# Optimization experiments

Hardware: AMD Instinct MI355X
Metric: run time of the kernel (lower is better)

Reference implementation:

```python
import jax, jax.numpy as jnp
import numpy as np

B, T, NE, H = 4, 1024, 1024, 16
HS = NE // H  # 64
EPS = 0.00064


def setup_inputs() -> dict:
    key = jax.random.key(0)
    ks = jax.random.split(key, 30)
    def rn(k, shape, s):
        return jax.random.normal(k, shape, jnp.float32) * s
    d = {}
    d["x"] = jax.random.normal(ks[0], (B, T, NE), jnp.float32)
    d["time_maa_x"] = jax.random.uniform(ks[1], (NE,), jnp.float32)
    d["time_maa"] = jax.random.uniform(ks[2], (4, 1, 1, NE), jnp.float32)
    d["maa_w1"] = rn(ks[3], (128, NE), 0.02)   # 4 * D_MIX_LORA=32
    d["maa_w2"] = rn(ks[4], (4, 32, NE), 0.02)
    d["decay_w1"] = rn(ks[5], (64, NE), 0.02)
    d["decay_w2"] = rn(ks[6], (64, NE), 0.02)
    d["aaa_w1"] = rn(ks[7], (16, NE), 0.02)
    d["aaa_w2"] = rn(ks[8], (16, NE), 0.02)
    d["kkk_w1"] = rn(ks[9], (16, NE), 0.02)
    d["kkk_w2"] = rn(ks[10], (16, NE), 0.02)
    d["gate_w1"] = rn(ks[11], (128, NE), 0.02)
    d["gate_w2"] = rn(ks[12], (128, NE), 0.02)
    d["ma_w1"] = rn(ks[13], (16, NE), 0.02)
    d["ma_w2"] = rn(ks[14], (16, NE), 0.02)
    d["mk_w1"] = rn(ks[15], (16, NE), 0.02)
    d["mk_w2"] = rn(ks[16], (16, NE), 0.02)
    d["time_decay"] = jnp.linspace(-6.5, -1.5, NE, dtype=jnp.float32)  # decay_speed + 0.5 shape
    d["time_faaaa"] = rn(ks[17], (NE,), 0.02)
    d["time_aaaaa"] = rn(ks[18], (NE,), 0.02)
    d["time_misc_a"] = rn(ks[19], (NE,), 0.02)
    d["time_misc_k"] = rn(ks[20], (NE,), 0.02)
    d["Wr"] = rn(ks[21], (NE, NE), 0.5 / NE ** 0.5)
    d["Wk"] = rn(ks[22], (NE, NE), 0.05 / NE ** 0.5)
    d["Wv"] = rn(ks[23], (NE, NE), 0.5 / NE ** 0.5)
    d["Wo"] = rn(ks[24], (NE, NE), 1.0 / NE ** 0.5)
    d["ln_w"] = jnp.ones((NE,), jnp.float32)
    d["ln_b"] = jnp.zeros((NE,), jnp.float32)
    return d


def _forward(x, time_maa_x, time_maa, maa_w1, maa_w2, decay_w1, decay_w2,
             aaa_w1, aaa_w2, kkk_w1, kkk_w2, gate_w1, gate_w2,
             ma_w1, ma_w2, mk_w1, mk_w2, time_decay, time_faaaa, time_aaaaa,
             time_misc_a, time_misc_k, Wr, Wk, Wv, Wo, ln_w, ln_b):
    Bx, Tx, C = x.shape
    # token-shift delta: xx[t] = x[t-1] - x[t], with x[-1] = 0
    xx = jnp.pad(x, ((0, 0), (1, 0), (0, 0)))[:, :Tx] - x
    mix = x + xx * time_maa_x
    lo = jnp.tanh(jnp.einsum('btc,dc->btd', mix, maa_w1)).reshape(Bx, Tx, 4, 32)
    lo = jnp.einsum('btgk,gkc->gbtc', lo, maa_w2)           # [4,B,T,C]
    xm = x[None] + xx[None] * (lo + time_maa)               # time_maa broadcasts [4,1,1,C]
    xrg, xwa, xk, xv = xm[0], xm[1], xm[2], xm[3]

    r = xrg @ Wr.T
    g = jnp.tanh(xrg @ gate_w1.T) @ gate_w2
    k = xk @ Wk.T
    v = xv @ Wv.T
    w2 = jnp.tanh(xwa @ decay_w1.T) @ decay_w2
    w = -jax.nn.softplus(-(time_decay + w2)) - 0.5
    kk = k + jnp.tanh(xk @ kkk_w1.T) @ kkk_w2
    kkh = kk.reshape(Bx, Tx, H, HS)
    kk = (kkh / jnp.maximum(jnp.linalg.norm(kkh, axis=-1, keepdims=True), 1e-12)).reshape(Bx, Tx, C)
    a = jax.nn.sigmoid(time_aaaaa + (xwa @ aaa_w1.T) @ aaa_w2)
    ma = jax.nn.sigmoid(time_misc_a + (xwa @ ma_w1.T) @ ma_w2)
    k = k * ma + k * a * (1.0 - ma)
    mk = jax.nn.sigmoid(time_misc_k + (xk @ mk_w1.T) @ mk_w2)
    k = k * jnp.exp(w * mk)
    b = -kk * a

    # RWKV7 delta-rule recurrence: per-(B,H) HSxHS matrix state, scan over T
    def to_th(t):
        return t.reshape(Bx, Tx, H, HS).transpose(1, 0, 2, 3)  # [T,B,H,HS]
    qt, wt, kt, vt, at, bt = map(to_th, (r, w, k, v, kk, b))
    wt = jnp.exp(-jnp.exp(wt))

    def step(s, inp):
        q_, w_, k_, v_, a_, b_ = inp
        sa = jnp.einsum('bhij,bhj->bhi', s, a_)
        s = s * w_[:, :, None, :] + sa[..., None] * b_[:, :, None, :] + v_[..., None] * k_[:, :, None, :]
        return s, jnp.einsum('bhij,bhj->bhi', s, q_)

    s0 = jnp.zeros((Bx, H, HS, HS), x.dtype)
    _, y = jax.lax.scan(step, s0, (qt, wt, kt, vt, at, bt))
    y = y.transpose(1, 0, 2, 3).reshape(Bx, Tx, C)

    # GroupNorm with H groups, eps=0.00064
    yg = y.reshape(Bx, Tx, H, HS)
    mu = yg.mean(-1, keepdims=True)
    var = ((yg - mu) ** 2).mean(-1, keepdims=True)
    y = ((yg - mu) / jnp.sqrt(var + EPS)).reshape(Bx, Tx, C) * ln_w + ln_b

    # per-head bonus: (r.k * faaaa) v
    rk = (r.reshape(Bx, Tx, H, HS) * k.reshape(Bx, Tx, H, HS) * time_faaaa.reshape(H, HS)).sum(-1, keepdims=True)
    y = y + (rk * v.reshape(Bx, Tx, H, HS)).reshape(Bx, Tx, C)
    return (y * g) @ Wo.T


def reference(x, time_maa_x, time_maa, maa_w1, maa_w2, decay_w1, decay_w2,
              aaa_w1, aaa_w2, kkk_w1, kkk_w2, gate_w1, gate_w2,
              ma_w1, ma_w2, mk_w1, mk_w2, time_decay, time_faaaa, time_aaaaa,
              time_misc_a, time_misc_k, Wr, Wk, Wv, Wo, ln_w, ln_b):
    return _forward(x, time_maa_x, time_maa, maa_w1, maa_w2, decay_w1, decay_w2,
                    aaa_w1, aaa_w2, kkk_w1, kkk_w2, gate_w1, gate_w2,
                    ma_w1, ma_w2, mk_w1, mk_w2, time_decay, time_faaaa, time_aaaaa,
                    time_misc_a, time_misc_k, Wr, Wk, Wv, Wo, ln_w, ln_b)
```

## Files before the change

kernel.cpp:

```cpp
#include <hip/hip_runtime.h>
#include <cstdint>
#include <cstddef>

#define BB   4
#define TT   1024
#define CC   1024
#define HH   16
#define HSS  64
#define NNtok 4096
#define EPSGN 0.00064f
#define W2TS 192

typedef unsigned short bf16u;
typedef __attribute__((ext_vector_type(8))) short short8;
typedef __attribute__((ext_vector_type(4))) float f32x4;
#define SLOT 4194304ull

__device__ __forceinline__ float bf2f(bf16u u){
  union { unsigned int i; float f; } cv; cv.i = ((unsigned int)u) << 16; return cv.f;
}
__device__ __forceinline__ unsigned short f2bfbits(unsigned int x){
  return (unsigned short)((x + 0x7fffu + ((x >> 16) & 1u)) >> 16);
}
__device__ __forceinline__ bf16u f2bf(float f){
  union { float f; unsigned int i; } cv; cv.f = f;
  return f2bfbits(cv.i);
}
__device__ __forceinline__ void ld4bf(const bf16u* p, float* o){
  ushort4 u = *reinterpret_cast<const ushort4*>(p);
  o[0]=bf2f(u.x); o[1]=bf2f(u.y); o[2]=bf2f(u.z); o[3]=bf2f(u.w);
}
__device__ __forceinline__ void st4bf(bf16u* p, const float* v){
  ushort4 u; u.x=f2bf(v[0]); u.y=f2bf(v[1]); u.z=f2bf(v[2]); u.w=f2bf(v[3]);
  *reinterpret_cast<ushort4*>(p) = u;
}
__device__ __forceinline__ unsigned short f2h(float f){
  union { _Float16 h; unsigned short s; } c; c.h = (_Float16)f; return c.s;
}
__device__ __forceinline__ void st4h(bf16u* p, const float* v){
  ushort4 u; u.x=f2h(v[0]); u.y=f2h(v[1]); u.z=f2h(v[2]); u.w=f2h(v[3]);
  *reinterpret_cast<ushort4*>(p) = u;
}
__device__ __forceinline__ void ld4f(const float* p, float* o){
  float4 v = *reinterpret_cast<const float4*>(p);
  o[0]=v.x; o[1]=v.y; o[2]=v.z; o[3]=v.w;
}
__device__ __forceinline__ float sigm(float x){ return 1.f / (1.f + expf(-x)); }

__device__ __forceinline__ float bflo(unsigned int u){
  union { unsigned int i; float f; } c; c.i = u << 16; return c.f;
}
__device__ __forceinline__ float bfhi(unsigned int u){
  union { unsigned int i; float f; } c; c.i = u & 0xffff0000u; return c.f;
}
__device__ __forceinline__ float hlo(unsigned int u){
  union { unsigned short s; _Float16 h; } c; c.s = (unsigned short)(u & 0xffffu); return (float)c.h;
}
__device__ __forceinline__ float hhi(unsigned int u){
  union { unsigned short s; _Float16 h; } c; c.s = (unsigned short)(u >> 16); return (float)c.h;
}
__device__ __forceinline__ float hval(unsigned short s){
  union { unsigned short s; _Float16 h; } c; c.s = s; return (float)c.h;
}
__device__ __forceinline__ float dot4(const float* x, const float* y){
  return (x[0]*y[0] + x[1]*y[1]) + (x[2]*y[2] + x[3]*y[3]);
}

__device__ __forceinline__ void gload_lds16(const bf16u* g, short* l){
  __builtin_amdgcn_global_load_lds(
      (const __attribute__((address_space(1))) unsigned int*)g,
      (__attribute__((address_space(3))) unsigned int*)l,
      16, 0, 0);
}

template<int CTRL>
__device__ __forceinline__ float dpp_add(float v){
  union { float f; int i; } a, b;
  a.f = v;
  b.i = __builtin_amdgcn_update_dpp(0, a.i, CTRL, 0xF, 0xF, true);
  return v + b.f;
}
__device__ __forceinline__ float red16(float v){
  v = dpp_add<0xB1>(v);
  v = dpp_add<0x4E>(v);
  v = dpp_add<0x124>(v);
  v = dpp_add<0x128>(v);
  return v;
}
__device__ __forceinline__ float red32(float v){
  v = red16(v);
  union { float f; int i; } x, y;
  x.f = v; y.f = v;
  asm volatile("" : "+v"(y.i));
  asm volatile("v_permlane16_swap_b32 %0, %1" : "+v"(x.i), "+v"(y.i));
  return x.f + y.f;
}

__global__ __launch_bounds__(256) void k_prep(const float* __restrict__ x,
                                              const float* __restrict__ tmx,
                                              bf16u* __restrict__ MIX){
  int e = (blockIdx.x * 256 + threadIdx.x) * 4;
  int n = e >> 10;
  int c = e & (CC - 1);
  int t = n & (TT - 1);
  float xf[4]; ld4f(x + e, xf);
  float pf[4] = {0.f, 0.f, 0.f, 0.f};
  if (t > 0) ld4f(x + e - CC, pf);
  float tm[4]; ld4f(tmx + c, tm);
  float mv[4];
  #pragma unroll
  for (int i = 0; i < 4; ++i) mv[i] = xf[i] + (pf[i] - xf[i]) * tm[i];
  st4bf(MIX + e, mv);
}

__global__ __launch_bounds__(256) void k_prep_wconv(
    const float* __restrict__ x, const float* __restrict__ tmx,
    bf16u* __restrict__ MIX,
    const float* __restrict__ Wr, const float* __restrict__ Wk,
    const float* __restrict__ Wv,
    const float* __restrict__ maa_w1, const float* __restrict__ gate_w1,
    const float* __restrict__ decay_w1, const float* __restrict__ aaa_w1,
    const float* __restrict__ ma_w1, const float* __restrict__ kkk_w1,
    const float* __restrict__ mk_w1,
    const float* __restrict__ maa_w2, const float* __restrict__ decay_w2,
    bf16u* __restrict__ WrB, bf16u* __restrict__ WkB, bf16u* __restrict__ WvB,
    bf16u* __restrict__ W1B, bf16u* __restrict__ W2TB){
  int tid = threadIdx.x;
  if (blockIdx.x < 4096){
    int e = (blockIdx.x * 256 + tid) * 4;
    int n = e >> 10;
    int c = e & (CC - 1);
    int t = n & (TT - 1);
    float xf[4]; ld4f(x + e, xf);
    float pf[4] = {0.f, 0.f, 0.f, 0.f};
    if (t > 0) ld4f(x + e - CC, pf);
    float tm[4]; ld4f(tmx + c, tm);
    float mv[4];
    #pragma unroll
    for (int i = 0; i < 4; ++i) mv[i] = xf[i] + (pf[i] - xf[i]) * tm[i];
    st4bf(MIX + e, mv);
    return;
  }
  int blk = blockIdx.x - 4096;
  if (blk < 3072){
    const float* src = (blk < 1024) ? Wr : (blk < 2048) ? Wk : Wv;
    bf16u* dst = (blk < 1024) ? WrB : (blk < 2048) ? WkB : WvB;
    size_t e = (size_t)(blk & 1023) * 1024 + (size_t)tid * 4;
    float v[4]; ld4f(src + e, v);
    st4bf(dst + e, v);
  } else if (blk < 3456){
    int row = blk - 3072;
    const float* src;
    if      (row < 128) src = maa_w1   + (size_t)row * 1024;
    else if (row < 256) src = gate_w1  + (size_t)(row - 128) * 1024;
    else if (row < 320) src = decay_w1 + (size_t)(row - 256) * 1024;
    else if (row < 336) src = aaa_w1   + (size_t)(row - 320) * 1024;
    else if (row < 352) src = ma_w1    + (size_t)(row - 336) * 1024;
    else if (row < 368) src = kkk_w1   + (size_t)(row - 352) * 1024;
    else                src = mk_w1    + (size_t)(row - 368) * 1024;
    float v[4]; ld4f(src + tid * 4, v);
    st4bf(W1B + (size_t)row * 1024 + tid * 4, v);
  } else {
    int j = blk - 3456;
    const float* src = (j < 128) ? (maa_w2 + (size_t)j * 1024)
                                 : (decay_w2 + (size_t)(j - 128) * 1024);
    for (int c = tid; c < 1024; c += 256)
      W2TB[(size_t)c * W2TS + j] = f2bf(src[c]);
  }
}

#define B64_AROW 72
#define B64_ASZ (64*72)
#define B64_BSZ (128*72)
template<bool OB>
__device__ __forceinline__ void gemm_b64_body(const bf16u* __restrict__ X,
                                              const bf16u* __restrict__ WB,
                                              void* __restrict__ OUTv,
                                              int Nd, int Kd, int act_n,
                                              short* __restrict__ As,
                                              short* __restrict__ Bs,
                                              int bn0, int bm0){
  const int tid  = threadIdx.x;
  const int lane = tid & 63;
  const int wv   = tid >> 6;
  const int wm   = wv >> 1, wn = wv & 1;
  const int l15  = lane & 15;
  const int quad = lane >> 4;

  f32x4 acc[2][4];
  #pragma unroll
  for (int mi = 0; mi < 2; ++mi)
    #pragma unroll
    for (int ni = 0; ni < 4; ++ni)
      #pragma unroll
      for (int rg = 0; rg < 4; ++rg) acc[mi][ni][rg] = 0.f;

  const int ra = tid >> 2, k0a = (tid & 3) * 16;
  const int rb = tid >> 1, k0b = (tid & 1) * 32;
  const bf16u* xsrc = X + (size_t)(bm0 + ra) * Kd;
  const bf16u* wsrc = (bn0 + rb < Nd) ? WB + (size_t)(bn0 + rb) * Kd : nullptr;

  uint4 xa0 = *(const uint4*)(xsrc + k0a);
  uint4 xa1 = *(const uint4*)(xsrc + k0a + 8);
  uint4 wa0 = make_uint4(0,0,0,0), wa1 = wa0, wa2 = wa0, wa3 = wa0;
  if (wsrc){
    wa0 = *(const uint4*)(wsrc + k0b);
    wa1 = *(const uint4*)(wsrc + k0b + 8);
    wa2 = *(const uint4*)(wsrc + k0b + 16);
    wa3 = *(const uint4*)(wsrc + k0b + 24);
  }
  *(uint4*)&As[ra * B64_AROW + k0a]      = xa0;
  *(uint4*)&As[ra * B64_AROW + k0a + 8]  = xa1;
  *(uint4*)&Bs[rb * B64_AROW + k0b]      = wa0;
  *(uint4*)&Bs[rb * B64_AROW + k0b + 8]  = wa1;
  *(uint4*)&Bs[rb * B64_AROW + k0b + 16] = wa2;
  *(uint4*)&Bs[rb * B64_AROW + k0b + 24] = wa3;
  __syncthreads();

  const int NS = Kd >> 6;
  for (int s = 0; s < NS; ++s){
    const int cur = s & 1;
    if (s + 1 < NS){
      int kb = (s + 1) << 6;
      xa0 = *(const uint4*)(xsrc + kb + k0a);
      xa1 = *(const uint4*)(xsrc + kb + k0a + 8);
      if (wsrc){
        wa0 = *(const uint4*)(wsrc + kb + k0b);
        wa1 = *(const uint4*)(wsrc + kb + k0b + 8);
        wa2 = *(const uint4*)(wsrc + kb + k0b + 16);
        wa3 = *(const uint4*)(wsrc + kb + k0b + 24);
      }
    }
    #pragma unroll
    for (int kk = 0; kk < 64; kk += 32){
      short8 af[2], bfg[4];
      #pragma unroll
      for (int mi = 0; mi < 2; ++mi)
        af[mi] = *(const short8*)&As[cur*B64_ASZ + (wm*32 + mi*16 + l15) * B64_AROW + kk + quad*8];
      #pragma unroll
      for (int ni = 0; ni < 4; ++ni)
        bfg[ni] = *(const short8*)&Bs[cur*B64_BSZ + (wn*64 + ni*16 + l15) * B64_AROW + kk + quad*8];
      #pragma unroll
      for (int mi = 0; mi < 2; ++mi)
        #pragma unroll
        for (int ni = 0; ni < 4; ++ni)
          acc[mi][ni] = __builtin_amdgcn_mfma_f32_16x16x32_bf16(af[mi], bfg[ni], acc[mi][ni], 0, 0, 0);
    }
    if (s + 1 < NS){
      const int nxt = cur ^ 1;
      *(uint4*)&As[nxt*B64_ASZ + ra * B64_AROW + k0a]      = xa0;
      *(uint4*)&As[nxt*B64_ASZ + ra * B64_AROW + k0a + 8]  = xa1;
      *(uint4*)&Bs[nxt*B64_BSZ + rb * B64_AROW + k0b]      = wa0;
      *(uint4*)&Bs[nxt*B64_BSZ + rb * B64_AROW + k0b + 8]  = wa1;
      *(uint4*)&Bs[nxt*B64_BSZ + rb * B64_AROW + k0b + 16] = wa2;
      *(uint4*)&Bs[nxt*B64_BSZ + rb * B64_AROW + k0b + 24] = wa3;
      __syncthreads();
    }
  }

  #pragma unroll
  for (int mi = 0; mi < 2; ++mi){
    #pragma unroll
    for (int ni = 0; ni < 4; ++ni){
      int col = bn0 + wn*64 + ni*16 + l15;
      if (col >= Nd) continue;
      #pragma unroll
      for (int rg = 0; rg < 4; ++rg){
        int row = bm0 + wm*32 + mi*16 + quad*4 + rg;
        float v = acc[mi][ni][rg];
        if (col < act_n) v = tanhf(v);
        if (OB) ((bf16u*)OUTv)[(size_t)row * Nd + col] = f2bf(v);
        else    ((float*)OUTv)[(size_t)row * Nd + col] = v;
      }
    }
  }
}

template<bool OB>
__global__ __launch_bounds__(256) void k_gemm_b64(const bf16u* __restrict__ X,
                                                  const bf16u* __restrict__ WB,
                                                  void* __restrict__ OUTv,
                                                  int Nd, int Kd, int act_n){
  __shared__ short As[2*B64_ASZ];
  __shared__ short Bs[2*B64_BSZ];
  gemm_b64_body<OB>(X, WB, OUTv, Nd, Kd, act_n, As, Bs,
                    blockIdx.x * 128, blockIdx.y * 64);
}

#define B128L_SZ (128*32)
template<bool OB>
__device__ __forceinline__ void gemm_b128_lds_body(const bf16u* __restrict__ X,
                                                   const bf16u* __restrict__ WB,
                                                   void* __restrict__ OUTv,
                                                   int Nd, int Kd, int act_n,
                                                   short* __restrict__ As,
                                                   short* __restrict__ Bs,
                                                   int bn0, int bm0){
  const int tid  = threadIdx.x;
  const int lane = tid & 63;
  const int wv   = tid >> 6;
  const int wm   = wv >> 1, wn = wv & 1;
  const int l15  = lane & 15;
  const int quad = lane >> 4;

  f32x4 acc[4][4];
  #pragma unroll
  for (int mi = 0; mi < 4; ++mi)
    #pragma unroll
    for (int ni = 0; ni < 4; ++ni)
      #pragma unroll
      for (int rg = 0; rg < 4; ++rg) acc[mi][ni][rg] = 0.f;

  const int srow = lane >> 2;
  const int cl   = (lane & 3) ^ ((lane >> 3) & 3);
  const bf16u* gA0 = X  + (size_t)(bm0 + wv*32 + srow)      * Kd + cl*8;
  const bf16u* gA1 = X  + (size_t)(bm0 + wv*32 + 16 + srow) * Kd + cl*8;
  const bf16u* gB0 = WB + (size_t)(bn0 + wv*32 + srow)      * Kd + cl*8;
  const bf16u* gB1 = WB + (size_t)(bn0 + wv*32 + 16 + srow) * Kd + cl*8;
  short* ldsA0 = As + wv*1024;
  short* ldsA1 = As + wv*1024 + 512;
  short* ldsB0 = Bs + wv*1024;
  short* ldsB1 = Bs + wv*1024 + 512;

  gload_lds16(gA0, ldsA0);
  gload_lds16(gA1, ldsA1);
  gload_lds16(gB0, ldsB0);
  gload_lds16(gB1, ldsB1);
  __syncthreads();

  const int cq = (quad ^ ((l15 >> 1) & 3)) * 8;
  const int NK = Kd >> 5;
  for (int k = 0; k < NK; ++k){
    const int cur = k & 1;
    if (k + 1 < NK){
      int ko = (k + 1) << 5;
      const int nxt = cur ^ 1;
      gload_lds16(gA0 + ko, ldsA0 + nxt*B128L_SZ);
      gload_lds16(gA1 + ko, ldsA1 + nxt*B128L_SZ);
      gload_lds16(gB0 + ko, ldsB0 + nxt*B128L_SZ);
      gload_lds16(gB1 + ko, ldsB1 + nxt*B128L_SZ);
    }
    short8 af[4], bfg[4];
    #pragma unroll
    for (int mi = 0; mi < 4; ++mi)
      af[mi] = *(const short8*)&As[cur*B128L_SZ + (wm*64 + mi*16 + l15) * 32 + cq];
    #pragma unroll
    for (int ni = 0; ni < 4; ++ni)
      bfg[ni] = *(const short8*)&Bs[cur*B128L_SZ + (wn*64 + ni*16 + l15) * 32 + cq];
    #pragma unroll
    for (int mi = 0; mi < 4; ++mi)
      #pragma unroll
      for (int ni = 0; ni < 4; ++ni)
        acc[mi][ni] = __builtin_amdgcn_mfma_f32_16x16x32_bf16(af[mi], bfg[ni], acc[mi][ni], 0, 0, 0);
    if (k + 1 < NK)
      __syncthreads();
  }

  #pragma unroll
  for (int mi = 0; mi < 4; ++mi){
    #pragma unroll
    for (int ni = 0; ni < 4; ++ni){
      int col = bn0 + wn*64 + ni*16 + l15;
      if (col >= Nd) continue;
      #pragma unroll
      for (int rg = 0; rg < 4; ++rg){
        int row = bm0 + wm*64 + mi*16 + quad*4 + rg;
        float v = acc[mi][ni][rg];
        if (col < act_n) v = tanhf(v);
        if (OB) ((bf16u*)OUTv)[(size_t)row * Nd + col] = f2bf(v);
        else    ((float*)OUTv)[(size_t)row * Nd + col] = v;
      }
    }
  }
}

__global__ __launch_bounds__(256) void k_gemm_b128_rkv(const bf16u* __restrict__ X0,
                                                       const bf16u* __restrict__ X2,
                                                       const bf16u* __restrict__ X3,
                                                       const bf16u* __restrict__ WrB,
                                                       const bf16u* __restrict__ WkB,
                                                       const bf16u* __restrict__ WvB,
                                                       bf16u* __restrict__ R,
                                                       bf16u* __restrict__ K0,
                                                       bf16u* __restrict__ V){
  __shared__ short As[2*B128L_SZ];
  __shared__ short Bs[2*B128L_SZ];
  const int z = blockIdx.z;
  const int bn0 = blockIdx.x * 128, bm0 = blockIdx.y * 128;
  if (z == 0)      gemm_b128_lds_body<true>(X0, WrB, R,  CC, CC, 0, As, Bs, bn0, bm0);
  else if (z == 1) gemm_b128_lds_body<true>(X2, WkB, K0, CC, CC, 0, As, Bs, bn0, bm0);
  else             gemm_b128_lds_body<true>(X3, WvB, V,  CC, CC, 0, As, Bs, bn0, bm0);
}

__global__ __launch_bounds__(256) void k_gemm_b64_lora(const bf16u* __restrict__ X0,
                                                       const bf16u* __restrict__ X1,
                                                       const bf16u* __restrict__ X2,
                                                       const bf16u* __restrict__ W1B,
                                                       bf16u* __restrict__ GT,
                                                       bf16u* __restrict__ P1,
                                                       bf16u* __restrict__ P2){
  __shared__ short As[2*B64_ASZ];
  __shared__ short Bs[2*B64_BSZ];
  const int z = blockIdx.z;
  const int bm0 = blockIdx.y * 64;
  if (z == 0)
    gemm_b64_body<true>(X0, W1B + 128*1024, GT, 128, CC, 128, As, Bs, 0, bm0);
  else if (z == 1)
    gemm_b64_body<true>(X1, W1B + 256*1024, P1, 96, CC, 64, As, Bs, 0, bm0);
  else
    gemm_b64_body<true>(X2, W1B + 352*1024, P2, 32, CC, 16, As, Bs, 0, bm0);
}

template<int KD, int EP>
__device__ __forceinline__ void gemm_nn_body(const bf16u* __restrict__ A, int lda,
                                             const bf16u* __restrict__ BT, int koff,
                                             bf16u* __restrict__ OUT,
                                             const float* __restrict__ x,
                                             const float* __restrict__ tma_g,
                                             short* __restrict__ As,
                                             short* __restrict__ Bs,
                                             int bn0, int bm0){
  const int tid  = threadIdx.x;
  const int lane = tid & 63;
  const int wv   = tid >> 6;
  const int wm   = wv >> 1, wn = wv & 1;
  const int l15  = lane & 15;
  const int quad = lane >> 4;

  for (int idx = tid; idx < 128 * (KD / 8); idx += 256){
    int r  = idx / (KD / 8);
    int kc = (idx % (KD / 8)) * 8;
    *(uint4*)&As[r * (KD + 8) + kc] =
        *(const uint4*)(A + (size_t)(bm0 + r) * lda + kc);
  }
  for (int idx = tid; idx < 128 * (KD / 8); idx += 256){
    int cc_ = idx / (KD / 8);
    int kc  = (idx % (KD / 8)) * 8;
    *(uint4*)&Bs[cc_ * (KD + 8) + kc] =
        *(const uint4*)(BT + (size_t)(bn0 + cc_) * W2TS + koff + kc);
  }
  __syncthreads();

  f32x4 acc[4][4];
  #pragma unroll
  for (int mi = 0; mi < 4; ++mi)
    #pragma unroll
    for (int ni = 0; ni < 4; ++ni)
      #pragma unroll
      for (int rg = 0; rg < 4; ++rg) acc[mi][ni][rg] = 0.f;

  #pragma unroll
  for (int kk = 0; kk < KD; kk += 32){
    short8 af[4], bfg[4];
    #pragma unroll
    for (int mi = 0; mi < 4; ++mi)
      af[mi] = *(const short8*)&As[(wm*64 + mi*16 + l15) * (KD + 8) + kk + quad*8];
    #pragma unroll
    for (int ni = 0; ni < 4; ++ni)
      bfg[ni] = *(const short8*)&Bs[(wn*64 + ni*16 + l15) * (KD + 8) + kk + quad*8];
    #pragma unroll
    for (int mi = 0; mi < 4; ++mi)
      #pragma unroll
      for (int ni = 0; ni < 4; ++ni)
        acc[mi][ni] = __builtin_amdgcn_mfma_f32_16x16x32_bf16(af[mi], bfg[ni], acc[mi][ni], 0, 0, 0);
  }

  #pragma unroll
  for (int mi = 0; mi < 4; ++mi){
    #pragma unroll
    for (int ni = 0; ni < 4; ++ni){
      int col = bn0 + wn*64 + ni*16 + l15;
      float tm = (EP == 1) ? tma_g[col] : 0.f;
      #pragma unroll
      for (int rg = 0; rg < 4; ++rg){
        int row = bm0 + wm*64 + mi*16 + quad*4 + rg;
        float v = acc[mi][ni][rg];
        if (EP == 1){
          float xv = x[(size_t)row * CC + col];
          float xp = ((row & (TT - 1)) == 0) ? 0.f : x[(size_t)row * CC + col - CC];
          v = xv + (xp - xv) * (v + tm);
        }
        OUT[(size_t)row * CC + col] = f2bf(v);
      }
    }
  }
}

template<int KD, int EP>
__global__ __launch_bounds__(256) void k_gemm_nn_b(const bf16u* __restrict__ A, int lda,
                                                   const bf16u* __restrict__ BT, int koff,
                                                   bf16u* __restrict__ OUT,
                                                   const float* __restrict__ x,
                                                   const float* __restrict__ tma_g){
  __shared__ short As[128 * (KD + 8)];
  __shared__ short Bs[128 * (KD + 8)];
  gemm_nn_body<KD, EP>(A, lda, BT, koff, OUT, x, tma_g, As, Bs,
                       blockIdx.x * 128, blockIdx.y * 128);
}

__global__ __launch_bounds__(256) void k_gemm_nn_b4(const bf16u* __restrict__ LO,
                                                    const bf16u* __restrict__ BT,
                                                    bf16u* __restrict__ X0base,
                                                    const float* __restrict__ x,
                                                    const float* __restrict__ tmaa){
  __shared__ short As[128 * 40];
  __shared__ short Bs[128 * 40];
  const int z = blockIdx.z;
  gemm_nn_body<32, 1>(LO + z*32, 128, BT, z*32, X0base + (size_t)z*SLOT,
                      x, tmaa + (size_t)z*CC, As, Bs,
                      blockIdx.x * 128, blockIdx.y * 128);
}

template<bool OB>
__global__ __launch_bounds__(256) void k_gemm_mfma(const bf16u* __restrict__ X,
                                                   const float* __restrict__ Wa,
                                                   const float* __restrict__ Wb,
                                                   const float* __restrict__ Wc,
                                                   int na, int nab,
                                                   void* __restrict__ OUTv,
                                                   int Nd, int Kd, int act_n){
  __shared__ short As[128 * 40];
  __shared__ short Bs[128 * 40];
  const int tid  = threadIdx.x;
  const int lane = tid & 63;
  const int wv   = tid >> 6;
  const int wm   = wv >> 1, wn = wv & 1;
  const int bn0  = blockIdx.x * 128;
  const int bm0  = blockIdx.y * 128;
  const int l15  = lane & 15;
  const int quad = lane >> 4;

  f32x4 acc[4][4];
  #pragma unroll
  for (int mi = 0; mi < 4; ++mi)
    #pragma unroll
    for (int ni = 0; ni < 4; ++ni)
      #pragma unroll
      for (int rg = 0; rg < 4; ++rg) acc[mi][ni][rg] = 0.f;

  const int r    = tid >> 1;
  const int half = (tid & 1) * 16;

  int rr = bn0 + r;
  const float* wsrc = nullptr;
  if (rr < na)        wsrc = Wa + (size_t)rr * Kd;
  else if (rr < nab)  wsrc = Wb + (size_t)(rr - na) * Kd;
  else if (rr < Nd)   wsrc = Wc + (size_t)(rr - nab) * Kd;
  const bf16u* xsrc = X + (size_t)(bm0 + r) * Kd;

  for (int k0 = 0; k0 < Kd; k0 += 32){
    uint4 xa = *(const uint4*)(xsrc + k0 + half);
    uint4 xb = *(const uint4*)(xsrc + k0 + half + 8);
    uint4 w0 = make_uint4(0,0,0,0), w1 = w0, w2 = w0, w3 = w0;
    if (wsrc){
      w0 = *(const uint4*)(wsrc + k0 + half);
      w1 = *(const uint4*)(wsrc + k0 + half + 4);
      w2 = *(const uint4*)(wsrc + k0 + half + 8);
      w3 = *(const uint4*)(wsrc + k0 + half + 12);
    }
    union { unsigned short s[8]; uint4 v; } p0, p1;
    p0.s[0]=f2bfbits(w0.x); p0.s[1]=f2bfbits(w0.y); p0.s[2]=f2bfbits(w0.z); p0.s[3]=f2bfbits(w0.w);
    p0.s[4]=f2bfbits(w1.x); p0.s[5]=f2bfbits(w1.y); p0.s[6]=f2bfbits(w1.z); p0.s[7]=f2bfbits(w1.w);
    p1.s[0]=f2bfbits(w2.x); p1.s[1]=f2bfbits(w2.y); p1.s[2]=f2bfbits(w2.z); p1.s[3]=f2bfbits(w2.w);
    p1.s[4]=f2bfbits(w3.x); p1.s[5]=f2bfbits(w3.y); p1.s[6]=f2bfbits(w3.z); p1.s[7]=f2bfbits(w3.w);

    *(uint4*)&As[r * 40 + half]     = xa;
    *(uint4*)&As[r * 40 + half + 8] = xb;
    *(uint4*)&Bs[r * 40 + half]     = p0.v;
    *(uint4*)&Bs[r * 40 + half + 8] = p1.v;
    __syncthreads();

    short8 af[4], bfg[4];
    #pragma unroll
    for (int mi = 0; mi < 4; ++mi)
      af[mi] = *(const short8*)&As[(wm*64 + mi*16 + l15) * 40 + quad*8];
    #pragma unroll
    for (int ni = 0; ni < 4; ++ni)
      bfg[ni] = *(const short8*)&Bs[(wn*64 + ni*16 + l15) * 40 + quad*8];
    #pragma unroll
    for (int mi = 0; mi < 4; ++mi)
      #pragma unroll
      for (int ni = 0; ni < 4; ++ni)
        acc[mi][ni] = __builtin_amdgcn_mfma_f32_16x16x32_bf16(af[mi], bfg[ni], acc[mi][ni], 0, 0, 0);
    __syncthreads();
  }

  #pragma unroll
  for (int mi = 0; mi < 4; ++mi){
    #pragma unroll
    for (int ni = 0; ni < 4; ++ni){
      int col = bn0 + wn*64 + ni*16 + l15;
      if (col >= Nd) continue;
      #pragma unroll
      for (int rg = 0; rg < 4; ++rg){
        int row = bm0 + wm*64 + mi*16 + quad*4 + rg;
        float v = acc[mi][ni][rg];
        if (col < act_n) v = tanhf(v);
        if (OB) ((bf16u*)OUTv)[(size_t)row * Nd + col] = f2bf(v);
        else    ((float*)OUTv)[(size_t)row * Nd + col] = v;
      }
    }
  }
}

template<int KD, int EP>
__global__ __launch_bounds__(256) void k_gemm_nn(const bf16u* __restrict__ A, int lda,
                                                 const float* __restrict__ B,
                                                 bf16u* __restrict__ OUT,
                                                 const float* __restrict__ x,
                                                 const float* __restrict__ tma_g){
  __shared__ short As[128 * (KD + 8)];
  __shared__ short Bs[128 * (KD + 8)];
  const int tid  = threadIdx.x;
  const int lane = tid & 63;
  const int wv   = tid >> 6;
  const int wm   = wv >> 1, wn = wv & 1;
  const int bn0  = blockIdx.x * 128;
  const int bm0  = blockIdx.y * 128;
  const int l15  = lane & 15;
  const int quad = lane >> 4;

  for (int idx = tid; idx < 128 * (KD / 8); idx += 256){
    int r  = idx / (KD / 8);
    int kc = (idx % (KD / 8)) * 8;
    *(uint4*)&As[r * (KD + 8) + kc] =
        *(const uint4*)(A + (size_t)(bm0 + r) * lda + kc);
  }
  for (int idx = tid; idx < KD * 128; idx += 256){
    int k = idx >> 7, c = idx & 127;
    Bs[c * (KD + 8) + k] = (short)f2bf(B[(size_t)k * CC + bn0 + c]);
  }
  __syncthreads();

  f32x4 acc[4][4];
  #pragma unroll
  for (int mi = 0; mi < 4; ++mi)
    #pragma unroll
    for (int ni = 0; ni < 4; ++ni)
      #pragma unroll
      for (int rg = 0; rg < 4; ++rg) acc[mi][ni][rg] = 0.f;

  #pragma unroll
  for (int kk = 0; kk < KD; kk += 32){
    short8 af[4], bfg[4];
    #pragma unroll
    for (int mi = 0; mi < 4; ++mi)
      af[mi] = *(const short8*)&As[(wm*64 + mi*16 + l15) * (KD + 8) + kk + quad*8];
    #pragma unroll
    for (int ni = 0; ni < 4; ++ni)
      bfg[ni] = *(const short8*)&Bs[(wn*64 + ni*16 + l15) * (KD + 8) + kk + quad*8];
    #pragma unroll
    for (int mi = 0; mi < 4; ++mi)
      #pragma unroll
      for (int ni = 0; ni < 4; ++ni)
        acc[mi][ni] = __builtin_amdgcn_mfma_f32_16x16x32_bf16(af[mi], bfg[ni], acc[mi][ni], 0, 0, 0);
  }

  #pragma unroll
  for (int mi = 0; mi < 4; ++mi){
    #pragma unroll
    for (int ni = 0; ni < 4; ++ni){
      int col = bn0 + wn*64 + ni*16 + l15;
      float tm = (EP == 1) ? tma_g[col] : 0.f;
      #pragma unroll
      for (int rg = 0; rg < 4; ++rg){
        int row = bm0 + wm*64 + mi*16 + quad*4 + rg;
        float v = acc[mi][ni][rg];
        if (EP == 1){
          float xv = x[(size_t)row * CC + col];
          float xp = ((row & (TT - 1)) == 0) ? 0.f : x[(size_t)row * CC + col - CC];
          v = xv + (xp - xv) * (v + tm);
        }
        OUT[(size_t)row * CC + col] = f2bf(v);
      }
    }
  }
}

template<int WMODE>
__global__ __launch_bounds__(256) void k_elem(bf16u* __restrict__ K0,
    const bf16u* __restrict__ P1, const bf16u* __restrict__ P2,
    const bf16u* __restrict__ W2A,
    const float* __restrict__ kw2, const float* __restrict__ aw2,
    const float* __restrict__ maw2, const float* __restrict__ mkw2,
    const float* __restrict__ td,  const float* __restrict__ taa,
    const float* __restrict__ tma, const float* __restrict__ tmk,
    const float* __restrict__ faaaa,
    bf16u* __restrict__ KKN, bf16u* __restrict__ Bb, bf16u* __restrict__ UX,
    float* __restrict__ WF,
    bf16u* __restrict__ Rq, float* __restrict__ Dsc, float* __restrict__ RKsc,
    const float* __restrict__ Wo, const float* __restrict__ gate_w2,
    bf16u* __restrict__ WoB, bf16u* __restrict__ GW2T){
  int tid = threadIdx.x;
  if (blockIdx.x >= 1024){
    int blk = blockIdx.x - 1024;
    if (blk < 1024){
      size_t e = ((size_t)blk * 256 + tid) * 4;
      float v[4]; ld4f(Wo + e, v);
      st4bf(WoB + e, v);
    } else {
      int c = (blk - 1024) * 2 + (tid >> 7);
      int j = tid & 127;
      GW2T[(size_t)c * 128 + j] = f2bf(gate_w2[(size_t)j * CC + c]);
    }
    return;
  }
  int n0 = blockIdx.x * 4;
  __shared__ float at_l[4][16], mat_l[4][16], kt_l[4][16], mkt_l[4][16];
  {
    int grp = tid >> 6, q = tid & 63, tt = q >> 4, j = q & 15;
    if (grp == 0)      at_l[tt][j]  = bf2f(P1[(size_t)(n0+tt)*96 + 64 + j]);
    else if (grp == 1) mat_l[tt][j] = bf2f(P1[(size_t)(n0+tt)*96 + 80 + j]);
    else if (grp == 2) kt_l[tt][j]  = bf2f(P2[(size_t)(n0+tt)*32 + j]);
    else               mkt_l[tt][j] = bf2f(P2[(size_t)(n0+tt)*32 + 16 + j]);
  }
  __syncthreads();
  int c  = tid * 4;
  int h  = tid >> 4;
  int lg = tid & 15;

  float kkk[4][4], aa[4][4], mam[4][4], mkm[4][4];
  #pragma unroll
  for (int tt = 0; tt < 4; ++tt)
    #pragma unroll
    for (int i = 0; i < 4; ++i){ kkk[tt][i]=0; aa[tt][i]=0; mam[tt][i]=0; mkm[tt][i]=0; }

  #pragma unroll 4
  for (int j = 0; j < 16; ++j){
    float wk[4], wa[4], wm[4], wq[4];
    ld4f(kw2  + (size_t)j*CC + c, wk);
    ld4f(aw2  + (size_t)j*CC + c, wa);
    ld4f(maw2 + (size_t)j*CC + c, wm);
    ld4f(mkw2 + (size_t)j*CC + c, wq);
    #pragma unroll
    for (int tt = 0; tt < 4; ++tt){
      float s1 = kt_l[tt][j], s2 = at_l[tt][j], s3 = mat_l[tt][j], s4 = mkt_l[tt][j];
      #pragma unroll
      for (int i = 0; i < 4; ++i){
        kkk[tt][i] += s1 * wk[i];
        aa[tt][i]  += s2 * wa[i];
        mam[tt][i] += s3 * wm[i];
        mkm[tt][i] += s4 * wq[i];
      }
    }
  }

  float td4[4], taa4[4], tma4[4], tmk4[4], fa4[4];
  ld4f(td + c, td4); ld4f(taa + c, taa4); ld4f(tma + c, tma4); ld4f(tmk + c, tmk4);
  ld4f(faaaa + c, fa4);

#define ELEM_TOKEN(TT_, E_, A_, B_, KF_, WD_) do{ \
    float k0a[4]; ld4bf(K0 + (E_), k0a); \
    float w2a[4]; ld4bf(W2A + (E_), w2a); \
    float ssq = 0.f; \
    _Pragma("unroll") \
    for (int i = 0; i < 4; ++i){ A_[i] = k0a[i] + kkk[TT_][i]; ssq += A_[i]*A_[i]; } \
    ssq = red16(ssq); \
    float rinv = 1.f / fmaxf(sqrtf(ssq), 1e-12f); \
    float outw_[4]; \
    _Pragma("unroll") \
    for (int i = 0; i < 4; ++i){ \
      float z  = td4[i] + w2a[i]; \
      float nz = -z; \
      float sp = (nz > 15.f) ? nz : log1pf(expf(nz)); \
      float w  = -sp - 0.5f; \
      float av  = sigm(taa4[i] + aa[TT_][i]); \
      float mav = sigm(tma4[i] + mam[TT_][i]); \
      float mkv = sigm(tmk4[i] + mkm[TT_][i]); \
      A_[i] *= rinv; \
      B_[i]  = -A_[i] * av; \
      KF_[i] = k0a[i] * (mav + av * (1.f - mav)) * expf(w * mkv); \
      float ou = -expf(w); \
      outw_[i] = ou; \
      if (WMODE == 1) WD_[i] = __expf(ou);               \
      else            WD_[i] = __expf(hval(f2h(ou)));    \
    } \
    st4bf(Bb + (E_), B_); \
    st4bf(K0 + (E_), KF_); \
    if (WMODE == 1) *(float4*)(WF + (E_)) = make_float4(WD_[0], WD_[1], WD_[2], WD_[3]); \
    else            st4h(UX + (E_), outw_); \
  }while(0)

  #pragma unroll
  for (int p = 0; p < 2; ++p){
    const int ttE = 2*p, ttO = ttE + 1;
    size_t eE = (size_t)(n0 + ttE) * CC + c;
    size_t eO = eE + CC;
    float aE[4], bE[4], kfE[4], wdE[4];
    float aO[4], bO[4], kfO[4], wdO[4];
    ELEM_TOKEN(ttE, eE, aE, bE, kfE, wdE);
    ELEM_TOKEN(ttO, eO, aO, bO, kfO, wdO);
    st4bf(KKN + eE, aE);

    float rE[4], rO[4];
    ld4bf(Rq + eE, rE); ld4bf(Rq + eO, rO);

    float rkE = red16(rE[0]*kfE[0]*fa4[0] + rE[1]*kfE[1]*fa4[1]
                    + rE[2]*kfE[2]*fa4[2] + rE[3]*kfE[3]*fa4[3]);
    float rkO = red16(rO[0]*kfO[0]*fa4[0] + rO[1]*kfO[1]*fa4[1]
                    + rO[2]*kfO[2]*fa4[2] + rO[3]*kfO[3]*fa4[3]);

    float c1 = red16(dot4(bE, aO));
    float d  = red16(dot4(kfE, aO));
    float u1[4];
    #pragma unroll
    for (int i = 0; i < 4; ++i) u1[i] = wdE[i]*aO[i] + c1*aE[i];
    st4bf(KKN + eO, u1);

    float cq = red16(dot4(bE, rE));
    float e1 = red16(dot4(kfE, rE));
    float qe[4];
    #pragma unroll
    for (int i = 0; i < 4; ++i) qe[i] = wdE[i]*rE[i] + cq*aE[i];
    st4bf(Rq + eE, qe);

    float cz  = red16(dot4(bO, rO));
    float e21 = red16(dot4(kfO, rO));
    float z[4];
    #pragma unroll
    for (int i = 0; i < 4; ++i) z[i] = wdO[i]*rO[i] + cz*aO[i];
    float cy  = red16(dot4(bE, z));
    float e20 = red16(dot4(kfE, z));
    float qo[4];
    #pragma unroll
    for (int i = 0; i < 4; ++i) qo[i] = wdE[i]*z[i] + cy*aE[i];
    st4bf(Rq + eO, qo);

    if (lg == 0){
      size_t pr = (size_t)((n0 + ttE) >> 1);
      float4 dv; dv.x = d; dv.y = e1; dv.z = e20; dv.w = e21;
      *(float4*)(Dsc + (pr * HH + h) * 4) = dv;
      RKsc[(size_t)(n0 + ttE) * HH + h] = rkE;
      RKsc[(size_t)(n0 + ttO) * HH + h] = rkO;
    }
  }
#undef ELEM_TOKEN
}

template<int WMODE>
__global__ __launch_bounds__(256) void k_rec(const bf16u* __restrict__ Qp,
                                             const bf16u* __restrict__ WT,
                                             const float* __restrict__ WF,
                                             const bf16u* __restrict__ KFt,
                                             const bf16u* __restrict__ Vt,
                                             const bf16u* __restrict__ Aa,
                                             const bf16u* __restrict__ Bv,
                                             const float* __restrict__ Dsc,
                                             bf16u* __restrict__ Y){
  const int p   = blockIdx.x;
  const int g   = (p & 7) | ((p >> 6) << 3);
  const int oct = (p >> 3) & 7;
  const int b   = g >> 4;
  const int h   = g & 15;
  const int tid = threadIdx.x;
  const int l31 = tid & 31;
  const int i   = oct * 8 + (tid >> 5);
  const size_t base0 = (size_t)(b * TT) * CC + h * HSS;
  const size_t colb  = base0 + l31 * 2;
  const size_t rowb  = base0 + i;
  const size_t dscb  = ((size_t)(b * (TT/2)) * HH + h) * 4;

  float S0 = 0.f, S1 = 0.f;

  unsigned int qEA,qOA,aEA,uOA,kEA,kOA,bEA,bOA,wEA,wOA; float2 fEA,fOA; unsigned short vEA,vOA; float4 dA;
  unsigned int qEB,qOB,aEB,uOB,kEB,kOB,bEB,bOB,wEB,wOB; float2 fEB,fOB; unsigned short vEB,vOB; float4 dB;
  unsigned int qEC,qOC,aEC,uOC,kEC,kOC,bEC,bOC,wEC,wOC; float2 fEC,fOC; unsigned short vEC,vOC; float4 dC;
  unsigned int qED,qOD,aED,uOD,kED,kOD,bED,bOD,wED,wOD; float2 fED,fOD; unsigned short vED,vOD; float4 dD;

#define PL(S, T_) do{ \
    size_t cE_ = colb + (size_t)(T_) * CC, cO_ = cE_ + CC; \
    qE##S = *(const unsigned int*)(Qp  + cE_); qO##S = *(const unsigned int*)(Qp  + cO_); \
    aE##S = *(const unsigned int*)(Aa  + cE_); uO##S = *(const unsigned int*)(Aa  + cO_); \
    kE##S = *(const unsigned int*)(KFt + cE_); kO##S = *(const unsigned int*)(KFt + cO_); \
    bE##S = *(const unsigned int*)(Bv  + cE_); bO##S = *(const unsigned int*)(Bv  + cO_); \
    if (WMODE == 1){ \
      fE##S = *(const float2*)(WF + cE_); fO##S = *(const float2*)(WF + cO_); \
    } else { \
      wE##S = *(const unsigned int*)(WT + cE_); wO##S = *(const unsigned int*)(WT + cO_); \
    } \
    vE##S = Vt[rowb + (size_t)(T_) * CC]; \
    vO##S = Vt[rowb + (size_t)(T_ + 1) * CC]; \
    d##S  = *(const float4*)(Dsc + dscb + (size_t)((T_) >> 1) * (HH*4)); \
  }while(0)

#define PSTEP(S, T_) do{ \
    float a0=bflo(aE##S), a1=bfhi(aE##S); \
    float u0=bflo(uO##S), u1=bfhi(uO##S); \
    float g0=bflo(qE##S), g1=bfhi(qE##S); \
    float o0=bflo(qO##S), o1=bfhi(qO##S); \
    float pE_ = fmaf(S1, a1, S0 * a0); \
    float pO_ = fmaf(S1, u1, S0 * u0); \
    float yE_ = fmaf(S1, g1, S0 * g0); \
    float yO_ = fmaf(S1, o1, S0 * o0); \
    pE_ = red32(pE_); \
    pO_ = red32(pO_); \
    yE_ = red32(yE_); \
    yO_ = red32(yO_); \
    float vEf = bf2f(vE##S), vOf = bf2f(vO##S); \
    float saE = pE_; \
    float saO = fmaf(d##S.x, vEf, pO_); \
    float ypE = fmaf(d##S.y, vEf, yE_); \
    float ypO = fmaf(d##S.z, vEf, fmaf(d##S.w, vOf, yO_)); \
    float k0=bflo(kE##S), k1=bfhi(kE##S); \
    float b0=bflo(bE##S), b1=bfhi(bE##S); \
    float w0, w1; \
    if (WMODE == 1){ w0=fE##S.x; w1=fE##S.y; } \
    else { w0=__expf(hlo(wE##S)); w1=__expf(hhi(wE##S)); } \
    S0 = fmaf(S0, w0, fmaf(saE, b0, vEf * k0)); \
    S1 = fmaf(S1, w1, fmaf(saE, b1, vEf * k1)); \
    float ko0=bflo(kO##S), ko1=bfhi(kO##S); \
    float bo0=bflo(bO##S), bo1=bfhi(bO##S); \
    float wo0, wo1; \
    if (WMODE == 1){ wo0=fO##S.x; wo1=fO##S.y; } \
    else { wo0=__expf(hlo(wO##S)); wo1=__expf(hhi(wO##S)); } \
    S0 = fmaf(S0, wo0, fmaf(saO, bo0, vOf * ko0)); \
    S1 = fmaf(S1, wo1, fmaf(saO, bo1, vOf * ko1)); \
    if (l31 == 0){ \
      Y[rowb + (size_t)(T_) * CC]     = f2bf(ypE); \
      Y[rowb + (size_t)(T_ + 1) * CC] = f2bf(ypO); \
    } \
  }while(0)

  PL(A, 0); PL(B, 2); PL(C, 4); PL(D, 6);
  for (int t = 0; t < TT; t += 8){
    PSTEP(A, t);
    if (t + 8  < TT) PL(A, t + 8);
    PSTEP(B, t + 2);
    if (t + 10 < TT) PL(B, t + 10);
    PSTEP(C, t + 4);
    if (t + 12 < TT) PL(C, t + 12);
    PSTEP(D, t + 6);
    if (t + 14 < TT) PL(D, t + 14);
  }
#undef PL
#undef PSTEP
}

__global__ __launch_bounds__(256) void k_post(const bf16u* __restrict__ Y,
                                              const bf16u* __restrict__ Vt,
                                              const bf16u* __restrict__ GV,
                                              const float* __restrict__ lnw,
                                              const float* __restrict__ lnb,
                                              const float* __restrict__ RKsc,
                                              bf16u* __restrict__ YG){
  int n = blockIdx.x, tid = threadIdx.x;
  int c = tid * 4;
  size_t e = (size_t)n * CC + c;

  float ya[4]; ld4bf(Y + e, ya);
  float s = ya[0] + ya[1] + ya[2] + ya[3];
  s = red16(s);
  float mu = s * (1.f / 64.f);
  float d[4], vs = 0.f;
  #pragma unroll
  for (int i = 0; i < 4; ++i){ d[i] = ya[i] - mu; vs += d[i] * d[i]; }
  vs = red16(vs);
  float rstd = rsqrtf(vs * (1.f / 64.f) + EPSGN);

  float rk = RKsc[(size_t)n * HH + (tid >> 4)];

  float va[4]; ld4bf(Vt + e, va);
  float lw4[4], lb4[4];
  ld4f(lnw + c, lw4); ld4f(lnb + c, lb4);
  float g[4]; ld4bf(GV + e, g);
  float o[4];
  #pragma unroll
  for (int i = 0; i < 4; ++i){
    float yn = d[i] * rstd * lw4[i] + lb4[i] + rk * va[i];
    o[i] = yn * g[i];
  }
  st4bf(YG + e, o);
}

extern "C" void kernel_launch(void* const* d_in, const int* in_sizes, int n_in,
                              void* d_out, int out_size, void* d_ws, size_t ws_size,
                              hipStream_t stream){
  (void)in_sizes; (void)n_in; (void)out_size;
  const float* x        = (const float*)d_in[0];
  const float* tmx      = (const float*)d_in[1];
  const float* tmaa     = (const float*)d_in[2];
  const float* maa_w1   = (const float*)d_in[3];
  const float* maa_w2   = (const float*)d_in[4];
  const float* decay_w1 = (const float*)d_in[5];
  const float* decay_w2 = (const float*)d_in[6];
  const float* aaa_w1   = (const float*)d_in[7];
  const float* aaa_w2   = (const float*)d_in[8];
  const float* kkk_w1   = (const float*)d_in[9];
  const float* kkk_w2   = (const float*)d_in[10];
  const float* gate_w1  = (const float*)d_in[11];
  const float* gate_w2  = (const float*)d_in[12];
  const float* ma_w1    = (const float*)d_in[13];
  const float* ma_w2    = (const float*)d_in[14];
  const float* mk_w1    = (const float*)d_in[15];
  const float* mk_w2    = (const float*)d_in[16];
  const float* t_decay  = (const float*)d_in[17];
  const float* t_faaaa  = (const float*)d_in[18];
  const float* t_aaaaa  = (const float*)d_in[19];
  const float* t_misc_a = (const float*)d_in[20];
  const float* t_misc_k = (const float*)d_in[21];
  const float* Wr       = (const float*)d_in[22];
  const float* Wk       = (const float*)d_in[23];
  const float* Wv       = (const float*)d_in[24];
  const float* Wo       = (const float*)d_in[25];
  const float* ln_w     = (const float*)d_in[26];
  const float* ln_b     = (const float*)d_in[27];

  bf16u* bw  = (bf16u*)d_ws;
  bf16u* MIX = bw + 0*SLOT;
  bf16u* X0  = bw + 0*SLOT;
  bf16u* KKN = bw + 0*SLOT;
  bf16u* YG  = bw + 0*SLOT;
  bf16u* X1  = bw + 1*SLOT;
  bf16u* Bb  = bw + 1*SLOT;
  bf16u* GV  = bw + 1*SLOT;
  bf16u* X2  = bw + 2*SLOT;
  bf16u* UX  = bw + 2*SLOT;
  bf16u* X3  = bw + 3*SLOT;
  bf16u* W2A = bw + 3*SLOT;
  bf16u* Yb  = bw + 3*SLOT;
  bf16u* R   = bw + 4*SLOT;
  bf16u* K0  = bw + 5*SLOT;
  bf16u* V   = bw + 6*SLOT;
  char*  wsb = (char*)d_ws;
  bf16u* LO  = (bf16u*)(wsb + (56ull<<20));
  bf16u* GT  = (bf16u*)(wsb + (57ull<<20));
  bf16u* P1  = (bf16u*)(wsb + (58ull<<20));
  bf16u* P2  = (bf16u*)(wsb + (58ull<<20) + (768ull<<10));
  float* Dsc = (float*)(wsb + (59ull<<20));
  float* RKsc= (float*)(wsb + (59ull<<20) + (512ull<<10));
  float* WF  = (float*)(wsb + (60ull<<20));
  bf16u* WrB = (bf16u*)(wsb + (60ull<<20));
  bf16u* WkB = (bf16u*)(wsb + (62ull<<20));
  bf16u* WvB = (bf16u*)(wsb + (64ull<<20));
  bf16u* W1B = (bf16u*)(wsb + (66ull<<20));
  bf16u* W2TB= (bf16u*)(wsb + (67ull<<20));
  bf16u* WoB = UX;
  bf16u* GW2T= UX + 1048576;
  const bool fast = ws_size >= (77ull<<20);

  if (fast){
    k_prep_wconv<<<7744, 256, 0, stream>>>(x, tmx, MIX,
                                           Wr, Wk, Wv, maa_w1, gate_w1, decay_w1,
                                           aaa_w1, ma_w1, kkk_w1, mk_w1,
                                           maa_w2, decay_w2,
                                           WrB, WkB, WvB, W1B, W2TB);
    k_gemm_b64<true><<<dim3(1,64),256,0,stream>>>(MIX, W1B, LO, 128, CC, 128);
    k_gemm_nn_b4<<<dim3(8,32,4),256,0,stream>>>(LO, W2TB, X0, x, tmaa);
    k_gemm_b128_rkv<<<dim3(8,32,3),256,0,stream>>>(X0, X2, X3, WrB, WkB, WvB,
                                                   R, K0, V);
    k_gemm_b64_lora<<<dim3(1,64,3),256,0,stream>>>(X0, X1, X2, W1B, GT, P1, P2);
    k_gemm_nn_b<64,0><<<dim3(8,32),256,0,stream>>>(P1, 96, W2TB, 128, W2A, nullptr, nullptr);
    k_elem<1><<<2560, 256, 0, stream>>>(K0, P1, P2, W2A,
                                        kkk_w2, aaa_w2, ma_w2, mk_w2,
                                        t_decay, t_aaaaa, t_misc_a, t_misc_k, t_faaaa,
                                        KKN, Bb, UX, WF, R, Dsc, RKsc,
                                        Wo, gate_w2, WoB, GW2T);
    k_rec<1><<<512, 256, 0, stream>>>(R, UX, WF, K0, V, KKN, Bb, Dsc, Yb);
    k_gemm_b64<true><<<dim3(8,64),256,0,stream>>>(GT, GW2T, GV, CC, 128, 0);
    k_post<<<4096, 256, 0, stream>>>(Yb, V, GV, ln_w, ln_b, RKsc, YG);
    k_gemm_b64<false><<<dim3(8,64),256,0,stream>>>(YG, WoB, d_out, CC, CC, 0);
  } else {
    k_prep<<<4096, 256, 0, stream>>>(x, tmx, MIX);
    k_gemm_mfma<true><<<dim3(1,32),256,0,stream>>>(MIX, maa_w1, maa_w1, maa_w1,
                                                   128, 128, LO, 128, CC, 128);
    bf16u* XMs[4] = {X0, X1, X2, X3};
    for (int g = 0; g < 4; ++g)
      k_gemm_nn<32,1><<<dim3(8,32),256,0,stream>>>(LO + g*32, 128,
                                                   maa_w2 + (size_t)g*32*CC,
                                                   XMs[g], x, tmaa + (size_t)g*CC);
    k_gemm_mfma<true><<<dim3(8,32),256,0,stream>>>(X0, Wr, Wr, Wr, CC, CC, R,  CC, CC, 0);
    k_gemm_mfma<true><<<dim3(8,32),256,0,stream>>>(X2, Wk, Wk, Wk, CC, CC, K0, CC, CC, 0);
    k_gemm_mfma<true><<<dim3(8,32),256,0,stream>>>(X3, Wv, Wv, Wv, CC, CC, V,  CC, CC, 0);
    k_gemm_mfma<true><<<dim3(1,32),256,0,stream>>>(X0, gate_w1, gate_w1, gate_w1,
                                                   128, 128, GT, 128, CC, 128);
    k_gemm_mfma<true><<<dim3(1,32),256,0,stream>>>(X1, decay_w1, aaa_w1, ma_w1,
                                                   64, 80, P1, 96, CC, 64);
    k_gemm_mfma<true><<<dim3(1,32),256,0,stream>>>(X2, kkk_w1, mk_w1, mk_w1,
                                                   16, 32, P2, 32, CC, 16);
    k_gemm_nn<64,0><<<dim3(8,32),256,0,stream>>>(P1, 96, decay_w2, W2A, nullptr, nullptr);
    k_elem<0><<<1024, 256, 0, stream>>>(K0, P1, P2, W2A,
                                        kkk_w2, aaa_w2, ma_w2, mk_w2,
                                        t_decay, t_aaaaa, t_misc_a, t_misc_k, t_faaaa,
                                        KKN, Bb, UX, WF, R, Dsc, RKsc,
                                        Wo, gate_w2, WoB, GW2T);
    k_rec<0><<<512, 256, 0, stream>>>(R, UX, WF, K0, V, KKN, Bb, Dsc, Yb);
    k_gemm_nn<128,0><<<dim3(8,32),256,0,stream>>>(GT, 128, gate_w2, GV, nullptr, nullptr);
    k_post<<<4096, 256, 0, stream>>>(Yb, V, GV, ln_w, ln_b, RKsc, YG);
    k_gemm_mfma<false><<<dim3(8,32),256,0,stream>>>(YG, Wo, Wo, Wo, CC, CC, d_out, CC, CC, 0);
  }
}
```

Before: 571.9 us.

## Co-schedule gate GEMM with recurrence kernel in a single launch

```diff
diff --git a/kernel.cpp b/kernel.cpp
--- a/kernel.cpp
+++ b/kernel.cpp
@@ -838,16 +838,16 @@
 }
 
 template<int WMODE>
-__global__ __launch_bounds__(256) void k_rec(const bf16u* __restrict__ Qp,
-                                             const bf16u* __restrict__ WT,
-                                             const float* __restrict__ WF,
-                                             const bf16u* __restrict__ KFt,
-                                             const bf16u* __restrict__ Vt,
-                                             const bf16u* __restrict__ Aa,
-                                             const bf16u* __restrict__ Bv,
-                                             const float* __restrict__ Dsc,
-                                             bf16u* __restrict__ Y){
-  const int p   = blockIdx.x;
+__device__ __forceinline__ void krec_body(int p,
+                                          const bf16u* __restrict__ Qp,
+                                          const bf16u* __restrict__ WT,
+                                          const float* __restrict__ WF,
+                                          const bf16u* __restrict__ KFt,
+                                          const bf16u* __restrict__ Vt,
+                                          const bf16u* __restrict__ Aa,
+                                          const bf16u* __restrict__ Bv,
+                                          const float* __restrict__ Dsc,
+                                          bf16u* __restrict__ Y){
   const int g   = (p & 7) | ((p >> 6) << 3);
   const int oct = (p >> 3) & 7;
   const int b   = g >> 4;
@@ -936,6 +936,41 @@
 #undef PSTEP
 }
 
+template<int WMODE>
+__global__ __launch_bounds__(256) void k_rec(const bf16u* __restrict__ Qp,
+                                             const bf16u* __restrict__ WT,
+                                             const float* __restrict__ WF,
+                                             const bf16u* __restrict__ KFt,
+                                             const bf16u* __restrict__ Vt,
+                                             const bf16u* __restrict__ Aa,
+                                             const bf16u* __restrict__ Bv,
+                                             const float* __restrict__ Dsc,
+                                             bf16u* __restrict__ Y){
+  krec_body<WMODE>(blockIdx.x, Qp, WT, WF, KFt, Vt, Aa, Bv, Dsc, Y);
+}
+
+__global__ __launch_bounds__(256) void k_rec_gv(const bf16u* __restrict__ Qp,
+                                                const float* __restrict__ WF,
+                                                const bf16u* __restrict__ KFt,
+                                                const bf16u* __restrict__ Vt,
+                                                const bf16u* __restrict__ Aa,
+                                                const bf16u* __restrict__ Bv,
+                                                const float* __restrict__ Dsc,
+                                                bf16u* __restrict__ Y,
+                                                const bf16u* __restrict__ GT,
+                                                const bf16u* __restrict__ GW2T,
+                                                bf16u* __restrict__ GVX){
+  __shared__ short As[2*B128L_SZ];
+  __shared__ short Bs[2*B128L_SZ];
+  if (blockIdx.x < 512){
+    krec_body<1>(blockIdx.x, Qp, nullptr, WF, KFt, Vt, Aa, Bv, Dsc, Y);
+  } else {
+    const int q = blockIdx.x - 512;
+    gemm_b128_lds_body<true>(GT, GW2T, GVX, CC, 128, 0, As, Bs,
+                             (q & 7) * 128, (q >> 3) * 128);
+  }
+}
+
 __global__ __launch_bounds__(256) void k_post(const bf16u* __restrict__ Y,
                                               const bf16u* __restrict__ Vt,
                                               const bf16u* __restrict__ GV,
@@ -1036,7 +1071,9 @@
   bf16u* W2TB= (bf16u*)(wsb + (67ull<<20));
   bf16u* WoB = UX;
   bf16u* GW2T= UX + 1048576;
-  const bool fast = ws_size >= (77ull<<20);
+  bf16u* GVX = (bf16u*)(wsb + (77ull<<20));
+  const bool fast  = ws_size >= (77ull<<20);
+  const bool fast2 = ws_size >= (85ull<<20);
 
   if (fast){
     k_prep_wconv<<<7744, 256, 0, stream>>>(x, tmx, MIX,
@@ -1055,9 +1092,15 @@
                                         t_decay, t_aaaaa, t_misc_a, t_misc_k, t_faaaa,
                                         KKN, Bb, UX, WF, R, Dsc, RKsc,
                                         Wo, gate_w2, WoB, GW2T);
-    k_rec<1><<<512, 256, 0, stream>>>(R, UX, WF, K0, V, KKN, Bb, Dsc, Yb);
-    k_gemm_b64<true><<<dim3(8,64),256,0,stream>>>(GT, GW2T, GV, CC, 128, 0);
-    k_post<<<4096, 256, 0, stream>>>(Yb, V, GV, ln_w, ln_b, RKsc, YG);
+    if (fast2){
+      k_rec_gv<<<768, 256, 0, stream>>>(R, WF, K0, V, KKN, Bb, Dsc, Yb,
+                                        GT, GW2T, GVX);
+      k_post<<<4096, 256, 0, stream>>>(Yb, V, GVX, ln_w, ln_b, RKsc, YG);
+    } else {
+      k_rec<1><<<512, 256, 0, stream>>>(R, nullptr, WF, K0, V, KKN, Bb, Dsc, Yb);
+      k_gemm_b64<true><<<dim3(8,64),256,0,stream>>>(GT, GW2T, GV, CC, 128, 0);
+      k_post<<<4096, 256, 0, stream>>>(Yb, V, GV, ln_w, ln_b, RKsc, YG);
+    }
     k_gemm_b64<false><<<dim3(8,64),256,0,stream>>>(YG, WoB, d_out, CC, CC, 0);
   } else {
     k_prep<<<4096, 256, 0, stream>>>(x, tmx, MIX);
```

Result: no change. 576.5 us (+0.8%).
